# Kernel optimization log

Measured on AMD Instinct MI355X. Metric: run time of the kernel, lower is better.

## Reference

```python
import jax, jax.numpy as jnp
import numpy as np

BETA_MIN = 0.1
BETA_MAX = 20.0

def _marginals(t):
    # VP-SDE closed forms: mean(t) = exp(-0.25 t^2 (bmax-bmin) - 0.5 t bmin), std = sqrt(1 - mean^2)
    log_mean = -0.25 * t ** 2 * (BETA_MAX - BETA_MIN) - 0.5 * t * BETA_MIN
    mean = jnp.exp(log_mean)
    std = jnp.sqrt(jnp.maximum(1.0 - jnp.exp(2.0 * log_mean), 1e-12))
    return mean, std

def setup_inputs() -> dict:
    key = jax.random.key(0)
    k1, k2, k3 = jax.random.split(key, 3)
    N, M, D = 4096, 16384, 128
    x = jax.random.normal(k1, (N, D), dtype=jnp.float32)
    t = jax.random.uniform(k2, (N,), dtype=jnp.float32, minval=0.05, maxval=1.0)
    train_data = jax.random.normal(k3, (M, D), dtype=jnp.float32)
    return {"x": x, "t": t, "train_data": train_data}

def reference(x, t, train_data):
    # x: (N, D), t: (N,), train_data: (M, D)
    mean, sigma = _marginals(t)                       # (N,), (N,)
    inv_var = 1.0 / (sigma ** 2)                      # (N,)
    # logpdf[n, i] = -0.5 * ||x_n - mean_n * y_i||^2 / sigma_n^2
    # expanded: ||x_n||^2 - 2 mean_n <x_n, y_i> + mean_n^2 ||y_i||^2
    xy = jnp.einsum('nd,md->nm', x, train_data)       # (N, M) GEMM
    x2 = jnp.sum(x ** 2, axis=1)                      # (N,)
    y2 = jnp.sum(train_data ** 2, axis=1)             # (M,)
    sq = x2[:, None] - 2.0 * mean[:, None] * xy + (mean ** 2)[:, None] * y2[None, :]
    logpdf = -0.5 * sq * inv_var[:, None]             # (N, M)
    weights = jax.nn.softmax(logpdf, axis=1)          # (N, M)
    evals = weights @ train_data                      # (N, D)
    evals = jnp.where(jnp.isnan(evals), 0.0, evals)
    return (evals - x) * inv_var[:, None]
```

## Files before the change

### kernel.cpp

```cpp
#include <hip/hip_runtime.h>

typedef unsigned int u32;
typedef unsigned short u16;
typedef short s16x8 __attribute__((ext_vector_type(8)));
typedef float f32x4 __attribute__((ext_vector_type(4)));

#define BETA_MIN 0.1f
#define BETA_MAX 20.0f

#define MFMA16(a, b, c) __builtin_amdgcn_mfma_f32_16x16x32_bf16(a, b, c, 0, 0, 0)

__device__ __forceinline__ u16 f2bf(float f) {
    u32 u = __float_as_uint(f);
    u32 r = u + 0x7FFFu + ((u >> 16) & 1u);
    return (u16)(r >> 16);
}
__device__ __forceinline__ float bf2f(u16 h) {
    return __uint_as_float(((u32)h) << 16);
}
__device__ __forceinline__ f32x4 zero4() {
    f32x4 z = {0.f, 0.f, 0.f, 0.f};
    return z;
}

template <int CTRL>
__device__ __forceinline__ float dppf(float x) {
    return __int_as_float(__builtin_amdgcn_update_dpp(
        0, __float_as_int(x), CTRL, 0xF, 0xF, false));
}
__device__ __forceinline__ float rowmax16(float x) {
    x = fmaxf(x, dppf<0xB1>(x));
    x = fmaxf(x, dppf<0x4E>(x));
    x = fmaxf(x, dppf<0x124>(x));
    x = fmaxf(x, dppf<0x128>(x));
    return x;
}
__device__ __forceinline__ float rowsum16(float x) {
    x += dppf<0xB1>(x);
    x += dppf<0x4E>(x);
    x += dppf<0x124>(x);
    x += dppf<0x128>(x);
    return x;
}


__global__ void conv_x_rows(const float* __restrict__ src, const float* __restrict__ t,
                            u16* __restrict__ hi, u16* __restrict__ lo,
                            float* __restrict__ rowc, int total4, int N) {
    int idx = blockIdx.x * blockDim.x + threadIdx.x;
    if (idx < N) {
        float tv   = t[idx];
        float lm   = -0.25f * tv * tv * (BETA_MAX - BETA_MIN) - 0.5f * tv * BETA_MIN;
        float mean = __expf(lm);
        float e2   = __expf(2.0f * lm);
        float s2   = fmaxf(1.0f - e2, 1e-12f);
        float iv   = 1.0f / s2;
        rowc[idx * 4 + 0] = mean * iv;
        rowc[idx * 4 + 1] = -0.5f * mean * mean * iv;
        rowc[idx * 4 + 2] = iv;
        rowc[idx * 4 + 3] = 0.f;
    }
    if (idx >= total4) return;
    float4 v = ((const float4*)src)[idx];
    float f[4] = {v.x, v.y, v.z, v.w};
    u32 hp[2], lp[2];
    u16 h[4], l[4];
#pragma unroll
    for (int j = 0; j < 4; ++j) {
        h[j] = f2bf(f[j]);
        l[j] = f2bf(f[j] - bf2f(h[j]));
    }
    hp[0] = (u32)h[0] | ((u32)h[1] << 16);
    hp[1] = (u32)h[2] | ((u32)h[3] << 16);
    lp[0] = (u32)l[0] | ((u32)l[1] << 16);
    lp[1] = (u32)l[2] | ((u32)l[3] << 16);
    ((uint2*)hi)[idx] = make_uint2(hp[0], hp[1]);
    ((uint2*)lo)[idx] = make_uint2(lp[0], lp[1]);
}

__global__ __launch_bounds__(256)
void train_prep_kernel(const float* __restrict__ train, u16* __restrict__ Khi,
                       u16* __restrict__ Klo, u16* __restrict__ Vt,
                       float* __restrict__ y2, int M) {
    __shared__ u16 T[128][66];
    const int t = threadIdx.x;
    const int m0 = blockIdx.x * 64;
    const int g = t >> 5, ln = t & 31;
#pragma unroll
    for (int i = 0; i < 8; ++i) {
        int lr = i * 8 + g;
        int m  = m0 + lr;
        const float* row = train + (size_t)m * 128;
        u16* kh = Khi + (size_t)m * 128;
        u16* kl = Klo + (size_t)m * 128;
        float acc = 0.f;
#pragma unroll
        for (int j = 0; j < 4; ++j) {
            int d = ln + 32 * j;
            float v = row[d];
            u16 h = f2bf(v);
            u16 l = f2bf(v - bf2f(h));
            T[d][lr] = h;
            kh[d] = h;
            kl[d] = l;
            acc += v * v;
        }
#pragma unroll
        for (int d = 16; d >= 1; d >>= 1) acc += __shfl_xor(acc, d, 32);
        if (ln == 0) y2[m] = acc;
    }
    __syncthreads();
#pragma unroll
    for (int i = 0; i < 4; ++i) {
        int c = i * 256 + t;
        int d = c >> 3, mo = (c & 7) * 8;
        u32 w0 = *(const u32*)&T[d][mo + 0];
        u32 w1 = *(const u32*)&T[d][mo + 2];
        u32 w2 = *(const u32*)&T[d][mo + 4];
        u32 w3 = *(const u32*)&T[d][mo + 6];
        *(uint4*)(Vt + (size_t)d * M + m0 + mo) = make_uint4(w0, w1, w2, w3);
    }
}

__global__ __launch_bounds__(512, 4)
void flash_kernel(const u16* __restrict__ Khi, const u16* __restrict__ Klo,
                  const u16* __restrict__ Vt,  const u16* __restrict__ Qhi,
                  const u16* __restrict__ Qlo, const float* __restrict__ rowc,
                  const float* __restrict__ y2, float* __restrict__ partO,
                  float* __restrict__ partML, int N, int M, int mchunk) {
    __shared__ u16 sKhi[32][136];
    __shared__ u16 sKlo[32][136];
    __shared__ u16 sVt[128][40];
    __shared__ u16 sP[8][16][40];

    const int tid  = threadIdx.x;
    const int wave = tid >> 6, lane = tid & 63;
    const int l15  = lane & 15, quad = lane >> 4;
    const int chunk = blockIdx.x, qb = blockIdx.y;
    const int q0 = qb * 128 + wave * 16;
    const int m_begin = chunk * mchunk;

    s16x8 qh[4], ql[4];
    {
        int row = q0 + l15;
        const u16* ph = Qhi + (size_t)row * 128;
        const u16* pl = Qlo + (size_t)row * 128;
#pragma unroll
        for (int kb = 0; kb < 4; ++kb) {
            qh[kb] = *(const s16x8*)(ph + kb * 32 + quad * 8);
            ql[kb] = *(const s16x8*)(pl + kb * 32 + quad * 8);
        }
    }
    float av[4], bv[4];
#pragma unroll
    for (int k = 0; k < 4; ++k) {
        int r = q0 + quad * 4 + k;
        av[k] = rowc[r * 4 + 0];
        bv[k] = rowc[r * 4 + 1];
    }

    f32x4 O[8];
#pragma unroll
    for (int db = 0; db < 8; ++db) O[db] = zero4();
    float m_run[4], l_run[4];
#pragma unroll
    for (int k = 0; k < 4; ++k) { m_run[k] = -INFINITY; l_run[k] = 0.f; }

    for (int mt = 0; mt < mchunk; mt += 32) {
        const int m0 = m_begin + mt;
        __syncthreads();
        {
            int row = tid >> 4, col = (tid & 15) * 8;
            *(uint4*)&sKhi[row][col] = *(const uint4*)(Khi + (size_t)(m0 + row) * 128 + col);
            *(uint4*)&sKlo[row][col] = *(const uint4*)(Klo + (size_t)(m0 + row) * 128 + col);
            int dd = tid >> 2, mc = (tid & 3) * 8;
            *(uint4*)&sVt[dd][mc] = *(const uint4*)(Vt + (size_t)dd * M + m0 + mc);
        }
        __syncthreads();

        float y2v0 = y2[m0 + l15];
        float y2v1 = y2[m0 + 16 + l15];

        f32x4 S[2];
        S[0] = zero4(); S[1] = zero4();
#pragma unroll
        for (int kb = 0; kb < 4; ++kb) {
            s16x8 bh0 = *(const s16x8*)&sKhi[l15][kb * 32 + quad * 8];
            s16x8 bh1 = *(const s16x8*)&sKhi[16 + l15][kb * 32 + quad * 8];
            s16x8 bl0 = *(const s16x8*)&sKlo[l15][kb * 32 + quad * 8];
            s16x8 bl1 = *(const s16x8*)&sKlo[16 + l15][kb * 32 + quad * 8];
            S[0] = MFMA16(qh[kb], bh0, S[0]);
            S[0] = MFMA16(ql[kb], bh0, S[0]);
            S[0] = MFMA16(qh[kb], bl0, S[0]);
            S[1] = MFMA16(qh[kb], bh1, S[1]);
            S[1] = MFMA16(ql[kb], bh1, S[1]);
            S[1] = MFMA16(qh[kb], bl1, S[1]);
        }

#pragma unroll
        for (int k = 0; k < 4; ++k) {
            float s0 = av[k] * S[0][k] + bv[k] * y2v0;
            float s1 = av[k] * S[1][k] + bv[k] * y2v1;
            float rm    = rowmax16(fmaxf(s0, s1));
            float mnew  = fmaxf(m_run[k], rm);
            float alpha = __expf(m_run[k] - mnew);
            float p0 = __expf(s0 - mnew);
            float p1 = __expf(s1 - mnew);
            m_run[k] = mnew;
            l_run[k] = l_run[k] * alpha + (p0 + p1);
            sP[wave][quad * 4 + k][l15]      = f2bf(p0);
            sP[wave][quad * 4 + k][16 + l15] = f2bf(p1);
#pragma unroll
            for (int db = 0; db < 8; ++db) O[db][k] *= alpha;
        }
        asm volatile("s_waitcnt lgkmcnt(0)" ::: "memory");

        s16x8 pa = *(const s16x8*)&sP[wave][l15][quad * 8];
#pragma unroll
        for (int db = 0; db < 8; ++db) {
            s16x8 vb = *(const s16x8*)&sVt[db * 16 + l15][quad * 8];
            O[db] = MFMA16(pa, vb, O[db]);
        }
    }

#pragma unroll
    for (int db = 0; db < 8; ++db) {
#pragma unroll
        for (int k = 0; k < 4; ++k) {
            int row = q0 + quad * 4 + k;
            partO[((size_t)chunk * N + row) * 128 + db * 16 + l15] = O[db][k];
        }
    }
#pragma unroll
    for (int k = 0; k < 4; ++k) {
        float lsum = rowsum16(l_run[k]);
        if (l15 == 0) {
            int row = q0 + quad * 4 + k;
            partML[((size_t)chunk * N + row) * 2 + 0] = m_run[k];
            partML[((size_t)chunk * N + row) * 2 + 1] = lsum;
        }
    }
}

__global__ void combine_kernel(const float* __restrict__ partO, const float* __restrict__ partML,
                               const float* __restrict__ x, const float* __restrict__ rowc,
                               float* __restrict__ out, int N, int split) {
    int n = blockIdx.x, d = threadIdx.x;
    float Mx = -INFINITY;
    for (int c = 0; c < split; ++c)
        Mx = fmaxf(Mx, partML[((size_t)c * N + n) * 2]);
    float L = 0.f, acc = 0.f;
    for (int c = 0; c < split; ++c) {
        float w = __expf(partML[((size_t)c * N + n) * 2] - Mx);
        L   += w * partML[((size_t)c * N + n) * 2 + 1];
        acc += w * partO[((size_t)c * N + n) * 128 + d];
    }
    float evals = acc / L;
    if (evals != evals) evals = 0.f;
    float iv = rowc[n * 4 + 2];
    out[(size_t)n * 128 + d] = (evals - x[(size_t)n * 128 + d]) * iv;
}

extern "C" void kernel_launch(void* const* d_in, const int* in_sizes, int n_in,
                              void* d_out, int out_size, void* d_ws, size_t ws_size,
                              hipStream_t stream) {
    const float* x     = (const float*)d_in[0];
    const float* t     = (const float*)d_in[1];
    const float* train = (const float*)d_in[2];
    float* out = (float*)d_out;

    const int N = in_sizes[1];
    const int D = 128;
    const int M = in_sizes[2] / D;

    char* ws = (char*)d_ws;
    size_t off = 0;
    auto alloc = [&](size_t bytes) -> void* {
        void* p = ws + off;
        off = (off + bytes + 255) & ~(size_t)255;
        return p;
    };
    u16* Khi   = (u16*)alloc((size_t)M * D * 2);
    u16* Klo   = (u16*)alloc((size_t)M * D * 2);
    u16* Vt    = (u16*)alloc((size_t)M * D * 2);
    u16* Qhi   = (u16*)alloc((size_t)N * D * 2);
    u16* Qlo   = (u16*)alloc((size_t)N * D * 2);
    float* rowc = (float*)alloc((size_t)N * 16);
    float* y2   = (float*)alloc((size_t)M * 4);
    size_t base = off;
    size_t per  = (size_t)N * D * 4 + (size_t)N * 8 + 512;
    int split = 16;
    while (split > 1 && base + per * split > ws_size) split >>= 1;
    float* partO  = (float*)alloc((size_t)split * N * D * 4);
    float* partML = (float*)alloc((size_t)split * N * 8);

    conv_x_rows<<<(N * D / 4 + 255) / 256, 256, 0, stream>>>(x, t, Qhi, Qlo, rowc,
                                                             N * D / 4, N);
    train_prep_kernel<<<M / 64, 256, 0, stream>>>(train, Khi, Klo, Vt, y2, M);

    int mchunk = M / split;
    dim3 grid(split, N / 128);
    flash_kernel<<<grid, 512, 0, stream>>>(Khi, Klo, Vt, Qhi, Qlo, rowc, y2,
                                           partO, partML, N, M, mchunk);
    combine_kernel<<<N, 128, 0, stream>>>(partO, partML, x, rowc, out, N, split);
}
```

Baseline: 179.0 us.

## Double-buffer K/V tiles via direct global-to-LDS loads and merge prep kernels

The flash kernel now stages K (hi/lo) and V tiles into double-buffered LDS using global_load_lds, prefetching the next tile while computing the current one. It uses XOR-swizzled unpadded layouts to avoid bank conflicts and drops one of the two barriers per iteration. The two preprocessing kernels are also merged into one launch, with blocks split by index. This aims to hide global load latency and cut launch overhead, at the cost of more LDS, which may reduce occupancy.

```diff
diff --git a/kernel.cpp b/kernel.cpp
--- a/kernel.cpp
+++ b/kernel.cpp
@@ -21,6 +21,12 @@
 __device__ __forceinline__ f32x4 zero4() {
     f32x4 z = {0.f, 0.f, 0.f, 0.f};
     return z;
+}
+
+__device__ __forceinline__ void gload_lds16(const void* g, void* l) {
+    __builtin_amdgcn_global_load_lds(
+        (__attribute__((address_space(1))) void*)(void*)g,
+        (__attribute__((address_space(3))) void*)l, 16, 0, 0);
 }
 
 template <int CTRL>
@@ -43,49 +49,48 @@
     return x;
 }
 
-
-__global__ void conv_x_rows(const float* __restrict__ src, const float* __restrict__ t,
-                            u16* __restrict__ hi, u16* __restrict__ lo,
-                            float* __restrict__ rowc, int total4, int N) {
-    int idx = blockIdx.x * blockDim.x + threadIdx.x;
-    if (idx < N) {
-        float tv   = t[idx];
-        float lm   = -0.25f * tv * tv * (BETA_MAX - BETA_MIN) - 0.5f * tv * BETA_MIN;
-        float mean = __expf(lm);
-        float e2   = __expf(2.0f * lm);
-        float s2   = fmaxf(1.0f - e2, 1e-12f);
-        float iv   = 1.0f / s2;
-        rowc[idx * 4 + 0] = mean * iv;
-        rowc[idx * 4 + 1] = -0.5f * mean * mean * iv;
-        rowc[idx * 4 + 2] = iv;
-        rowc[idx * 4 + 3] = 0.f;
-    }
-    if (idx >= total4) return;
-    float4 v = ((const float4*)src)[idx];
-    float f[4] = {v.x, v.y, v.z, v.w};
-    u32 hp[2], lp[2];
-    u16 h[4], l[4];
-#pragma unroll
-    for (int j = 0; j < 4; ++j) {
-        h[j] = f2bf(f[j]);
-        l[j] = f2bf(f[j] - bf2f(h[j]));
-    }
-    hp[0] = (u32)h[0] | ((u32)h[1] << 16);
-    hp[1] = (u32)h[2] | ((u32)h[3] << 16);
-    lp[0] = (u32)l[0] | ((u32)l[1] << 16);
-    lp[1] = (u32)l[2] | ((u32)l[3] << 16);
-    ((uint2*)hi)[idx] = make_uint2(hp[0], hp[1]);
-    ((uint2*)lo)[idx] = make_uint2(lp[0], lp[1]);
-}
-
 __global__ __launch_bounds__(256)
-void train_prep_kernel(const float* __restrict__ train, u16* __restrict__ Khi,
-                       u16* __restrict__ Klo, u16* __restrict__ Vt,
-                       float* __restrict__ y2, int M) {
+void prep_kernel(const float* __restrict__ x, const float* __restrict__ t,
+                 const float* __restrict__ train,
+                 u16* __restrict__ Qhi, u16* __restrict__ Qlo, float* __restrict__ rowc,
+                 u16* __restrict__ Khi, u16* __restrict__ Klo, u16* __restrict__ Vt,
+                 float* __restrict__ y2, int total4, int N, int M, int nconvblk) {
     __shared__ u16 T[128][66];
-    const int t = threadIdx.x;
-    const int m0 = blockIdx.x * 64;
-    const int g = t >> 5, ln = t & 31;
+    if ((int)blockIdx.x < nconvblk) {
+        int idx = blockIdx.x * 256 + threadIdx.x;
+        if (idx < N) {
+            float tv   = t[idx];
+            float lm   = -0.25f * tv * tv * (BETA_MAX - BETA_MIN) - 0.5f * tv * BETA_MIN;
+            float mean = __expf(lm);
+            float e2   = __expf(2.0f * lm);
+            float s2   = fmaxf(1.0f - e2, 1e-12f);
+            float iv   = 1.0f / s2;
+            rowc[idx * 4 + 0] = mean * iv;
+            rowc[idx * 4 + 1] = -0.5f * mean * mean * iv;
+            rowc[idx * 4 + 2] = iv;
+            rowc[idx * 4 + 3] = 0.f;
+        }
+        if (idx >= total4) return;
+        float4 v = ((const float4*)x)[idx];
+        float f[4] = {v.x, v.y, v.z, v.w};
+        u32 hp[2], lp[2];
+        u16 h[4], l[4];
+#pragma unroll
+        for (int j = 0; j < 4; ++j) {
+            h[j] = f2bf(f[j]);
+            l[j] = f2bf(f[j] - bf2f(h[j]));
+        }
+        hp[0] = (u32)h[0] | ((u32)h[1] << 16);
+        hp[1] = (u32)h[2] | ((u32)h[3] << 16);
+        lp[0] = (u32)l[0] | ((u32)l[1] << 16);
+        lp[1] = (u32)l[2] | ((u32)l[3] << 16);
+        ((uint2*)Qhi)[idx] = make_uint2(hp[0], hp[1]);
+        ((uint2*)Qlo)[idx] = make_uint2(lp[0], lp[1]);
+        return;
+    }
+    const int tt = threadIdx.x;
+    const int m0 = (blockIdx.x - nconvblk) * 64;
+    const int g = tt >> 5, ln = tt & 31;
 #pragma unroll
     for (int i = 0; i < 8; ++i) {
         int lr = i * 8 + g;
@@ -112,7 +117,7 @@
     __syncthreads();
 #pragma unroll
     for (int i = 0; i < 4; ++i) {
-        int c = i * 256 + t;
+        int c = i * 256 + tt;
         int d = c >> 3, mo = (c & 7) * 8;
         u32 w0 = *(const u32*)&T[d][mo + 0];
         u32 w1 = *(const u32*)&T[d][mo + 2];
@@ -128,9 +133,8 @@
                   const u16* __restrict__ Qlo, const float* __restrict__ rowc,
                   const float* __restrict__ y2, float* __restrict__ partO,
                   float* __restrict__ partML, int N, int M, int mchunk) {
-    __shared__ u16 sKhi[32][136];
-    __shared__ u16 sKlo[32][136];
-    __shared__ u16 sVt[128][40];
+    __shared__ u16 sK[2][2][32][128];
+    __shared__ u16 sV[2][128][32];
     __shared__ u16 sP[8][16][40];
 
     const int tid  = threadIdx.x;
@@ -140,6 +144,21 @@
     const int q0 = qb * 128 + wave * 16;
     const int m_begin = chunk * mchunk;
 
+    const int kr = tid >> 4;
+    const int kc = (tid & 15) ^ (kr & 7);
+    const int vd = tid >> 2;
+    const int vc = (tid & 3) ^ ((vd >> 1) & 3);
+    const u16* gKh = Khi + (size_t)(m_begin + kr) * 128 + kc * 8;
+    const u16* gKl = Klo + (size_t)(m_begin + kr) * 128 + kc * 8;
+    const u16* gV  = Vt  + (size_t)vd * M + m_begin + vc * 8;
+    const int wb = wave * 1024;
+
+    int aK[4];
+#pragma unroll
+    for (int kb = 0; kb < 4; ++kb)
+        aK[kb] = l15 * 256 + ((((kb * 4 + quad) ^ (l15 & 7))) << 4);
+    const int aV = l15 * 64 + ((quad ^ ((l15 >> 1) & 3)) << 4);
+
     s16x8 qh[4], ql[4];
     {
         int row = q0 + l15;
@@ -166,29 +185,34 @@
 #pragma unroll
     for (int k = 0; k < 4; ++k) { m_run[k] = -INFINITY; l_run[k] = 0.f; }
 
+    auto stage = [&](int buf) {
+        gload_lds16(gKh, (char*)&sK[buf][0][0][0] + wb);
+        gload_lds16(gKl, (char*)&sK[buf][1][0][0] + wb);
+        gload_lds16(gV,  (char*)&sV[buf][0][0]    + wb);
+        gKh += 32 * 128; gKl += 32 * 128; gV += 32;
+    };
+
+    stage(0);
+    __syncthreads();
+    int cur = 0;
+
     for (int mt = 0; mt < mchunk; mt += 32) {
+        if (mt + 32 < mchunk) stage(cur ^ 1);
         const int m0 = m_begin + mt;
-        __syncthreads();
-        {
-            int row = tid >> 4, col = (tid & 15) * 8;
-            *(uint4*)&sKhi[row][col] = *(const uint4*)(Khi + (size_t)(m0 + row) * 128 + col);
-            *(uint4*)&sKlo[row][col] = *(const uint4*)(Klo + (size_t)(m0 + row) * 128 + col);
-            int dd = tid >> 2, mc = (tid & 3) * 8;
-            *(uint4*)&sVt[dd][mc] = *(const uint4*)(Vt + (size_t)dd * M + m0 + mc);
-        }
-        __syncthreads();
-
         float y2v0 = y2[m0 + l15];
         float y2v1 = y2[m0 + 16 + l15];
 
+        const char* Kb = (const char*)&sK[cur][0][0][0];
+        const char* Vb = (const char*)&sV[cur][0][0];
+
         f32x4 S[2];
         S[0] = zero4(); S[1] = zero4();
 #pragma unroll
         for (int kb = 0; kb < 4; ++kb) {
-            s16x8 bh0 = *(const s16x8*)&sKhi[l15][kb * 32 + quad * 8];
-            s16x8 bh1 = *(const s16x8*)&sKhi[16 + l15][kb * 32 + quad * 8];
-            s16x8 bl0 = *(const s16x8*)&sKlo[l15][kb * 32 + quad * 8];
-            s16x8 bl1 = *(const s16x8*)&sKlo[16 + l15][kb * 32 + quad * 8];
+            s16x8 bh0 = *(const s16x8*)(Kb + aK[kb]);
+            s16x8 bh1 = *(const s16x8*)(Kb + aK[kb] + 4096);
+            s16x8 bl0 = *(const s16x8*)(Kb + aK[kb] + 8192);
+            s16x8 bl1 = *(const s16x8*)(Kb + aK[kb] + 12288);
             S[0] = MFMA16(qh[kb], bh0, S[0]);
             S[0] = MFMA16(ql[kb], bh0, S[0]);
             S[0] = MFMA16(qh[kb], bl0, S[0]);
@@ -218,9 +242,11 @@
         s16x8 pa = *(const s16x8*)&sP[wave][l15][quad * 8];
 #pragma unroll
         for (int db = 0; db < 8; ++db) {
-            s16x8 vb = *(const s16x8*)&sVt[db * 16 + l15][quad * 8];
+            s16x8 vb = *(const s16x8*)(Vb + db * 1024 + aV);
             O[db] = MFMA16(pa, vb, O[db]);
         }
+        __syncthreads();
+        cur ^= 1;
     }
 
 #pragma unroll
@@ -294,9 +320,10 @@
     float* partO  = (float*)alloc((size_t)split * N * D * 4);
     float* partML = (float*)alloc((size_t)split * N * 8);
 
-    conv_x_rows<<<(N * D / 4 + 255) / 256, 256, 0, stream>>>(x, t, Qhi, Qlo, rowc,
-                                                             N * D / 4, N);
-    train_prep_kernel<<<M / 64, 256, 0, stream>>>(train, Khi, Klo, Vt, y2, M);
+    int nconvblk = (N * D / 4 + 255) / 256;
+    int nblk = nconvblk + M / 64;
+    prep_kernel<<<nblk, 256, 0, stream>>>(x, t, train, Qhi, Qlo, rowc,
+                                          Khi, Klo, Vt, y2, N * D / 4, N, M, nconvblk);
 
     int mchunk = M / split;
     dim3 grid(split, N / 128);
```

Result: faster. 174.2 us (-2.7%).
